# Optimization experiments

Measured on AMD Instinct MI355X. Metric: run time of the kernel, lower is better.

The kernel has to match this reference:

```python
import jax, jax.numpy as jnp
import numpy as np
from math import log

MODEL_DIM = 512
NUM_HEADS = 8
DIM_HEAD = 64
INNER = NUM_HEADS * DIM_HEAD
B, L = 8, 1024
EPS = 1e-5


def setup_inputs() -> dict:
    key = jax.random.key(0)
    ks = jax.random.split(key, 9)
    x = jax.random.normal(ks[0], (B, L, MODEL_DIM), dtype=jnp.float32)
    gamma = jnp.ones((MODEL_DIM,), jnp.float32)
    beta = jnp.zeros((MODEL_DIM,), jnp.float32)
    w_qkv = jax.random.normal(ks[1], (3 * INNER, MODEL_DIM), jnp.float32) * (MODEL_DIM ** -0.5)
    b_qkv = jnp.zeros((3 * INNER,), jnp.float32)
    w_pos = jax.random.normal(ks[2], (INNER, MODEL_DIM), jnp.float32) * (MODEL_DIM ** -0.5)
    w_out = jax.random.normal(ks[3], (MODEL_DIM, INNER), jnp.float32) * (INNER ** -0.5)
    b_out = jnp.zeros((MODEL_DIM,), jnp.float32)
    # xavier_uniform for (num_heads, dim_head)
    bound = (6.0 / (NUM_HEADS + DIM_HEAD)) ** 0.5
    u_bias = jax.random.uniform(ks[4], (NUM_HEADS, DIM_HEAD), jnp.float32, -bound, bound)
    v_bias = jax.random.uniform(ks[5], (NUM_HEADS, DIM_HEAD), jnp.float32, -bound, bound)
    return {"x": x, "gamma": gamma, "beta": beta, "w_qkv": w_qkv, "b_qkv": b_qkv,
            "w_pos": w_pos, "w_out": w_out, "b_out": b_out, "u_bias": u_bias, "v_bias": v_bias}


def _rel_pos_emb(seq_len, d):
    # (L, D): (i - j) scaled by sinusoid frequencies, then cos on even cols, sin on odd cols
    rel = (jnp.arange(seq_len, dtype=jnp.float32)[:, None]
           - jnp.arange(d, dtype=jnp.float32)[None, :])
    freqs = jnp.exp(-jnp.arange(0, 2 * d, 2, dtype=jnp.float32) * (log(10000.0) / MODEL_DIM))
    angle = rel * freqs[None, :]
    even = (jnp.arange(d) % 2) == 0
    return jnp.where(even[None, :], jnp.cos(angle), jnp.sin(angle))  # (L, D)


def reference(x, gamma, beta, w_qkv, b_qkv, w_pos, w_out, b_out, u_bias, v_bias):
    b, l, d = x.shape
    h, dh = NUM_HEADS, DIM_HEAD
    # LayerNorm
    mu = jnp.mean(x, axis=-1, keepdims=True)
    var = jnp.mean(jnp.square(x - mu), axis=-1, keepdims=True)
    xn = (x - mu) * jax.lax.rsqrt(var + EPS) * gamma + beta
    # relative position embedding, identical per batch element
    pe = _rel_pos_emb(l, d)                      # (L, D)
    pos = (pe @ w_pos.T).reshape(l, h, dh)       # (L, H, Dh)
    pos = jnp.transpose(pos, (1, 0, 2))          # (H, L, Dh)
    # qkv
    qkv = xn @ w_qkv.T + b_qkv                   # (B, L, 3*inner)
    q, k, v = jnp.split(qkv, 3, axis=-1)
    def to_heads(t):
        return jnp.transpose(t.reshape(b, l, h, dh), (0, 2, 1, 3))  # (B,H,L,Dh)
    q, k, v = to_heads(q), to_heads(k), to_heads(v)
    scale = dh ** -0.5
    content = jnp.einsum('bhld,bhmd->bhlm', q + u_bias[None, :, None, :], k)
    pos_score = jnp.einsum('bhld,hmd->bhlm', q + v_bias[None, :, None, :], pos)
    attn = jax.nn.softmax((content + pos_score) * scale, axis=-1)
    out = jnp.einsum('bhlm,bhmd->bhld', attn, v)
    out = jnp.transpose(out, (0, 2, 1, 3)).reshape(b, l, h * dh)
    return out @ w_out.T + b_out  # dropout p=0.0 -> identity
```

## Files before the change

### kernel.cpp

```cpp
#include <hip/hip_runtime.h>
#include <math.h>

static constexpr int Bn = 8, Ln = 1024, Dm = 512, Hn = 8, DhN = 64;

typedef short bf16x8 __attribute__((ext_vector_type(8)));
typedef float f32x4 __attribute__((ext_vector_type(4)));
typedef _Float16 f16x4 __attribute__((ext_vector_type(4)));
typedef _Float16 f16x8 __attribute__((ext_vector_type(8)));
typedef unsigned int u32x4 __attribute__((ext_vector_type(4)));

#define QSCALE 0.1803368801111137f

static __device__ __forceinline__ unsigned short f2b(float f) {
  union { float f; unsigned int u; } x;
  x.f = f;
  unsigned int u = x.u;
  unsigned int r = (u + 0x7FFFu + ((u >> 16) & 1u)) >> 16;
  return (unsigned short)r;
}
static __device__ __forceinline__ float b2f(unsigned short u) {
  union { unsigned int u; float f; } x;
  x.u = ((unsigned int)u) << 16;
  return x.f;
}

#define GLDS16(g, l)                                                        \
  __builtin_amdgcn_global_load_lds((const __attribute__((address_space(1))) void*)(g), \
                                   (__attribute__((address_space(3))) void*)(l), 16, 0, 0)

__global__ __launch_bounds__(256) void prep1(const float* __restrict__ x,
                                             const float* __restrict__ gamma,
                                             const float* __restrict__ beta,
                                             unsigned short* __restrict__ xn,
                                             unsigned short* __restrict__ pe,
                                             const float* __restrict__ wq, unsigned short* __restrict__ wqb,
                                             const float* __restrict__ wp, unsigned short* __restrict__ wpb,
                                             const float* __restrict__ wo, unsigned short* __restrict__ wob) {
  int b = blockIdx.x;
  int t = threadIdx.x;
  if (b < 8192) {
    const float2 v = *(const float2*)(x + (size_t)b * Dm + t * 2);
    float s = v.x + v.y;
    float sq = v.x * v.x + v.y * v.y;
#pragma unroll
    for (int off = 32; off > 0; off >>= 1) {
      s += __shfl_down(s, off);
      sq += __shfl_down(sq, off);
    }
    __shared__ float red[8];
    int wave = t >> 6, lane = t & 63;
    if (lane == 0) { red[wave * 2] = s; red[wave * 2 + 1] = sq; }
    __syncthreads();
    float S = red[0] + red[2] + red[4] + red[6];
    float SQ = red[1] + red[3] + red[5] + red[7];
    float mu = S * (1.0f / Dm);
    float var = SQ * (1.0f / Dm) - mu * mu;
    float rstd = rsqrtf(var + 1e-5f);
    int c = t * 2;
    ushort2 o;
    o.x = f2b((v.x - mu) * rstd * gamma[c] + beta[c]);
    o.y = f2b((v.y - mu) * rstd * gamma[c + 1] + beta[c + 1]);
    *(ushort2*)(xn + (size_t)b * Dm + c) = o;
  } else if (b < 10240) {
    int idx = (b - 8192) * 256 + t;
    int l = idx >> 9, k = idx & 511;
    float freq = expf(-0.0359778921f * (float)k);
    float angle = (float)(l - k) * freq;
    pe[idx] = f2b((k & 1) ? sinf(angle) : cosf(angle));
  } else {
    int cb = b - 10240;
    const float* src;
    unsigned short* dst;
    int off;
    if (cb < 768) { src = wq; dst = wqb; off = cb; }
    else if (cb < 1024) { src = wp; dst = wpb; off = cb - 768; }
    else { src = wo; dst = wob; off = cb - 1024; }
    int i = off * 256 + t;
    float4 v = *(const float4*)(src + (size_t)i * 4);
    ushort4 o;
    o.x = f2b(v.x); o.y = f2b(v.y); o.z = f2b(v.z); o.w = f2b(v.w);
    *(ushort4*)(dst + (size_t)i * 4) = o;
  }
}

__global__ __launch_bounds__(256, 8) void gemm_mfma(const unsigned short* __restrict__ Ain,
                                                    const unsigned short* __restrict__ Bwin,
                                                    const float* __restrict__ biasin,
                                                    float* __restrict__ outfin,
                                                    unsigned short* __restrict__ oq,
                                                    unsigned short* __restrict__ ok,
                                                    unsigned short* __restrict__ ov,
                                                    const unsigned short* __restrict__ A2,
                                                    const unsigned short* __restrict__ B2,
                                                    float* __restrict__ outf2,
                                                    int K, int mode) {
  int by = blockIdx.y, bx = blockIdx.x;
  if (by < 128) {
    int NBX = gridDim.x;
    int lid = by * NBX + bx;
    int i = lid >> 3;
    by = (lid & 7) * 16 + i / NBX;
    bx = i % NBX;
  }
  const unsigned short* A = Ain;
  const unsigned short* Bw = Bwin;
  const float* bias = biasin;
  float* outf = outfin;
  if (by >= 128) {
    if (bx >= 8) return;
    A = A2; Bw = B2; bias = nullptr; outf = outf2; mode = 1; by -= 128;
  }
  __shared__ alignas(16) unsigned short As[64 * 64];
  __shared__ alignas(16) unsigned short Bs[64 * 64];
  const int t = threadIdx.x;
  const int lane = t & 63, w = t >> 6;
  const int c = lane & 15, q8 = lane >> 4;
  const int wm = (w & 1) * 32, wn = (w >> 1) * 32;
  const int m0 = by * 64, n0 = bx * 64;

  f32x4 acc[2][2];
#pragma unroll
  for (int i = 0; i < 2; ++i)
#pragma unroll
    for (int j = 0; j < 2; ++j) acc[i][j] = (f32x4){0.f, 0.f, 0.f, 0.f};

  const int srow = lane >> 3;
  const int sgr = (lane & 7) ^ srow;

  for (int k0 = 0; k0 < K; k0 += 64) {
    __syncthreads();
#pragma unroll
    for (int j = 0; j < 2; ++j) {
      int r = j * 32 + w * 8 + srow;
      GLDS16(A + (size_t)(m0 + r) * K + k0 + sgr * 8, As + (j * 256 + w * 64 + lane) * 8);
      GLDS16(Bw + (size_t)(n0 + r) * K + k0 + sgr * 8, Bs + (j * 256 + w * 64 + lane) * 8);
    }
    __syncthreads();
#pragma unroll
    for (int kk = 0; kk < 2; ++kk) {
      bf16x8 a[2], b[2];
      const int q = kk * 4 + q8;
#pragma unroll
      for (int i = 0; i < 2; ++i) {
        int r = wm + i * 16 + c;
        a[i] = *(const bf16x8*)&As[(r * 8 + (q ^ (r & 7))) * 8];
      }
#pragma unroll
      for (int j = 0; j < 2; ++j) {
        int r = wn + j * 16 + c;
        b[j] = *(const bf16x8*)&Bs[(r * 8 + (q ^ (r & 7))) * 8];
      }
#pragma unroll
      for (int i = 0; i < 2; ++i)
#pragma unroll
        for (int j = 0; j < 2; ++j)
          acc[i][j] = __builtin_amdgcn_mfma_f32_16x16x32_bf16(a[i], b[j], acc[i][j], 0, 0, 0);
    }
  }
#pragma unroll
  for (int i = 0; i < 2; ++i) {
#pragma unroll
    for (int r = 0; r < 4; ++r) {
      int m = m0 + wm + i * 16 + q8 * 4 + r;
#pragma unroll
      for (int j = 0; j < 2; ++j) {
        int n = n0 + wn + j * 16 + c;
        float val = acc[i][j][r] + (bias ? bias[n] : 0.0f);
        if (mode == 0) {
          int part = n >> 9, h = (n >> 6) & 7, dh = n & 63;
          int bb = m >> 10, l = m & 1023;
          size_t idx = (size_t)((bb * 8 + h) * 1024 + l) * 64 + dh;
          if (part == 0) {
            oq[idx] = f2b(val * QSCALE);
          } else if (part == 1) {
            ok[idx] = f2b(val);
          } else {
            union { _Float16 h; unsigned short u; } cv;
            cv.h = (_Float16)val;
            ov[idx] = cv.u;
          }
        } else if (mode == 1) {
          int h = n >> 6, dh = n & 63;
          outf[(size_t)(h * 1024 + m) * 64 + dh] = val;
        } else {
          outf[(size_t)m * 512 + n] = val;
        }
      }
    }
  }
}

__global__ __launch_bounds__(256) void prep2(unsigned short* __restrict__ kbuf,
                                             const float* __restrict__ pos,
                                             const float* __restrict__ ub,
                                             const float* __restrict__ vbb,
                                             float* __restrict__ biasout,
                                             const unsigned short* __restrict__ v,
                                             unsigned short* __restrict__ vt) {
  int b = blockIdx.x;
  int t = threadIdx.x;
  if (b < 16384) {
    int wave = t >> 6, lane = t & 63;
    int g = b * 4 + wave;
    int h = (g >> 10) & 7;
    int m = g & 1023;
    float kv = b2f(kbuf[(size_t)g * 64 + lane]);
    float pv = pos[(size_t)(h * 1024 + m) * 64 + lane];
    float val = ub[h * 64 + lane] * kv + vbb[h * 64 + lane] * pv;
#pragma unroll
    for (int off = 32; off > 0; off >>= 1) val += __shfl_down(val, off);
    if (lane == 0) biasout[g] = val * QSCALE;
    kbuf[(size_t)g * 64 + lane] = f2b(kv + pv);
  } else {
    __shared__ unsigned short Ts[64 * 68];
    int bb = b - 16384;
    int bh = bb >> 4, lt = bb & 15;
    const unsigned short* vg = v + (size_t)bh * 65536 + lt * 4096;
#pragma unroll
    for (int s = 0; s < 4; ++s) {
      int idx = t + s * 256;
      int r = idx >> 4, c4 = (idx & 15) << 2;
      *(ushort4*)&Ts[r * 68 + c4] = *(const ushort4*)(vg + r * 64 + c4);
    }
    __syncthreads();
#pragma unroll
    for (int s = 0; s < 4; ++s) {
      int idx = t + s * 256;
      int d = idx >> 4, l4 = (idx & 15) << 2;
      ushort4 o;
      o.x = Ts[(l4 + 0) * 68 + d];
      o.y = Ts[(l4 + 1) * 68 + d];
      o.z = Ts[(l4 + 2) * 68 + d];
      o.w = Ts[(l4 + 3) * 68 + d];
      int pb = ((l4 >> 5) & 1) * 32 + ((l4 >> 2) & 3) * 8 + ((l4 >> 4) & 1) * 4;
      *(ushort4*)(vt + (size_t)bh * 65536 + d * 1024 + lt * 64 + pb) = o;
    }
  }
}

__global__ __launch_bounds__(256, 2) void flash_mfma(const unsigned short* __restrict__ qbf,
                                                     const unsigned short* __restrict__ kbf,
                                                     const unsigned short* __restrict__ vt,
                                                     const float* __restrict__ bias,
                                                     unsigned short* __restrict__ attn_out) {
  __shared__ alignas(16) unsigned short Ks[2][64 * 64];
  __shared__ alignas(16) unsigned short Vs[2][64 * 64];
  __shared__ alignas(16) float Bls[1024];
  const int t = threadIdx.x;
  const int lane = t & 63, w = t >> 6;
  const int c = lane & 15, q8 = lane >> 4;
  const int cc7 = c & 7;
  const int lid = blockIdx.x + (blockIdx.y << 3);
  const int bh = ((lid & 7) << 3) + ((lid >> 3) & 7);
  const int qt = lid >> 6;
  const unsigned short* qg = qbf + (size_t)bh * 65536;
  const unsigned short* kg = kbf + (size_t)bh * 65536;
  const unsigned short* vg = vt + (size_t)bh * 65536;
  const float* bg = bias + (size_t)bh * 1024;

  GLDS16(bg + t * 4, Bls + t * 4);

  bf16x8 bq[2][2];
#pragma unroll
  for (int g = 0; g < 2; ++g) {
    int qlg = qt * 128 + g * 64 + w * 16 + c;
    bq[g][0] = *(const bf16x8*)(qg + (size_t)qlg * 64 + q8 * 8);
    bq[g][1] = *(const bf16x8*)(qg + (size_t)qlg * 64 + 32 + q8 * 8);
  }

  float m_st[2] = {-INFINITY, -INFINITY};
  float l_st[2] = {0.0f, 0.0f};
  f32x4 o[2][4];
#pragma unroll
  for (int g = 0; g < 2; ++g)
#pragma unroll
    for (int i = 0; i < 4; ++i) o[g][i] = (f32x4){0.f, 0.f, 0.f, 0.f};

  const int srow = lane >> 3;
  const int sgr = (lane & 7) ^ srow;
  const int r0 = w * 16 + srow;

  u32x4 pk[2][2], pv[2][2];
#pragma unroll
  for (int h = 0; h < 2; ++h)
#pragma unroll
    for (int j = 0; j < 2; ++j) {
      int r = r0 + j * 8;
      pk[h][j] = *(const u32x4*)(kg + (size_t)(h * 64 + r) * 64 + sgr * 8);
      pv[h][j] = *(const u32x4*)(vg + (size_t)r * 1024 + h * 64 + sgr * 8);
    }

  for (int it = 0; it < 8; ++it) {
    __syncthreads();
#pragma unroll
    for (int h = 0; h < 2; ++h)
#pragma unroll
      for (int j = 0; j < 2; ++j) {
        int r = r0 + j * 8;
        *(u32x4*)&Ks[h][(r * 8 + (lane & 7)) * 8] = pk[h][j];
        *(u32x4*)&Vs[h][(r * 8 + (lane & 7)) * 8] = pv[h][j];
      }
    __syncthreads();
    if (it < 7) {
#pragma unroll
      for (int h = 0; h < 2; ++h)
#pragma unroll
        for (int j = 0; j < 2; ++j) {
          int r = r0 + j * 8;
          pk[h][j] = *(const u32x4*)(kg + (size_t)((it + 1) * 128 + h * 64 + r) * 64 + sgr * 8);
          pv[h][j] = *(const u32x4*)(vg + (size_t)r * 1024 + (it + 1) * 128 + h * 64 + sgr * 8);
        }
    }

    f32x4 sc[2][2][4];
#pragma unroll
    for (int h = 0; h < 2; ++h) {
#pragma unroll
      for (int nt = 0; nt < 4; ++nt) {
        f32x4 ci = *(const f32x4*)&Bls[it * 128 + h * 64 + nt * 16 + q8 * 4];
        const int row = nt * 16 + c;
        bf16x8 ak0 = *(const bf16x8*)&Ks[h][(row * 8 + (q8 ^ cc7)) * 8];
        bf16x8 ak1 = *(const bf16x8*)&Ks[h][(row * 8 + ((q8 + 4) ^ cc7)) * 8];
#pragma unroll
        for (int g = 0; g < 2; ++g) {
          f32x4 z = __builtin_amdgcn_mfma_f32_16x16x32_bf16(ak0, bq[g][0], ci, 0, 0, 0);
          sc[g][h][nt] = __builtin_amdgcn_mfma_f32_16x16x32_bf16(ak1, bq[g][1], z, 0, 0, 0);
        }
      }
    }
    float mx[2];
#pragma unroll
    for (int g = 0; g < 2; ++g) {
      float m = sc[g][0][0][0];
#pragma unroll
      for (int h = 0; h < 2; ++h)
#pragma unroll
        for (int nt = 0; nt < 4; ++nt)
#pragma unroll
          for (int r = 0; r < 4; ++r) m = fmaxf(m, sc[g][h][nt][r]);
      mx[g] = m;
    }
    {
      float s0 = __shfl_xor(mx[0], 16);
      float s1 = __shfl_xor(mx[1], 16);
      mx[0] = fmaxf(mx[0], s0);
      mx[1] = fmaxf(mx[1], s1);
      s0 = __shfl_xor(mx[0], 32);
      s1 = __shfl_xor(mx[1], 32);
      mx[0] = fmaxf(mx[0], s0);
      mx[1] = fmaxf(mx[1], s1);
    }
    f16x8 pf8[2][2][2];
#pragma unroll
    for (int g = 0; g < 2; ++g) {
      float mn = fmaxf(m_st[g], mx[g]);
      float al = __builtin_amdgcn_exp2f(m_st[g] - mn);
      float su = 0.0f;
#pragma unroll
      for (int h = 0; h < 2; ++h)
#pragma unroll
        for (int nt = 0; nt < 4; ++nt)
#pragma unroll
          for (int r = 0; r < 4; ++r) {
            float p = __builtin_amdgcn_exp2f(sc[g][h][nt][r] - mn);
            su += p;
            pf8[g][h][nt >> 1][((nt & 1) << 2) | r] = (_Float16)p;
          }
      l_st[g] = l_st[g] * al + su;
      m_st[g] = mn;
#pragma unroll
      for (int i = 0; i < 4; ++i) o[g][i] *= al;
    }
#pragma unroll
    for (int i = 0; i < 4; ++i) {
      const int row = i * 16 + c;
#pragma unroll
      for (int h = 0; h < 2; ++h) {
        f16x8 va = *(const f16x8*)&Vs[h][(row * 8 + (q8 ^ cc7)) * 8];
        f16x8 vb = *(const f16x8*)&Vs[h][(row * 8 + ((4 + q8) ^ cc7)) * 8];
#pragma unroll
        for (int g = 0; g < 2; ++g) {
          o[g][i] = __builtin_amdgcn_mfma_f32_16x16x32_f16(va, pf8[g][h][0], o[g][i], 0, 0, 0);
          o[g][i] = __builtin_amdgcn_mfma_f32_16x16x32_f16(vb, pf8[g][h][1], o[g][i], 0, 0, 0);
        }
      }
    }
  }
  float lt0 = l_st[0], lt1 = l_st[1];
  {
    float s0 = __shfl_xor(lt0, 16);
    float s1 = __shfl_xor(lt1, 16);
    lt0 += s0; lt1 += s1;
    s0 = __shfl_xor(lt0, 32);
    s1 = __shfl_xor(lt1, 32);
    lt0 += s0; lt1 += s1;
  }
  const int bidx = bh >> 3, h = bh & 7;
#pragma unroll
  for (int g = 0; g < 2; ++g) {
    int qlg = qt * 128 + g * 64 + w * 16 + c;
    float inv = 1.0f / (g == 0 ? lt0 : lt1);
    size_t base = (size_t)(bidx * 1024 + qlg) * 512 + h * 64;
#pragma unroll
    for (int i = 0; i < 4; ++i) {
      ushort4 ov4;
      ov4.x = f2b(o[g][i][0] * inv);
      ov4.y = f2b(o[g][i][1] * inv);
      ov4.z = f2b(o[g][i][2] * inv);
      ov4.w = f2b(o[g][i][3] * inv);
      *(ushort4*)(attn_out + base + i * 16 + q8 * 4) = ov4;
    }
  }
}

extern "C" void kernel_launch(void* const* d_in, const int* in_sizes, int n_in,
                              void* d_out, int out_size, void* d_ws, size_t ws_size,
                              hipStream_t stream) {
  const float* x      = (const float*)d_in[0];
  const float* gamma  = (const float*)d_in[1];
  const float* beta   = (const float*)d_in[2];
  const float* w_qkv  = (const float*)d_in[3];
  const float* b_qkv  = (const float*)d_in[4];
  const float* w_pos  = (const float*)d_in[5];
  const float* w_out  = (const float*)d_in[6];
  const float* b_out  = (const float*)d_in[7];
  const float* u_bias = (const float*)d_in[8];
  const float* v_bias = (const float*)d_in[9];
  float* out = (float*)d_out;

  unsigned short* wsu = (unsigned short*)d_ws;
  unsigned short* xnb   = wsu;
  unsigned short* peb   = wsu + 4194304;
  unsigned short* wqkvb = wsu + 4718592;
  unsigned short* wposb = wsu + 5505024;
  unsigned short* woutb = wsu + 5767168;
  unsigned short* qbf   = wsu + 6291456;
  unsigned short* kbf   = wsu + 10485760;
  unsigned short* vbf   = wsu + 14680064;
  unsigned short* vtb   = wsu + 18874368;
  unsigned short* attnb = wsu + 23068672;
  float* posb  = (float*)(wsu + 27262976);
  float* biasb = (float*)(wsu + 28311552);

  prep1<<<11520, 256, 0, stream>>>(x, gamma, beta, xnb, peb,
                                   w_qkv, wqkvb, w_pos, wposb, w_out, woutb);
  gemm_mfma<<<dim3(24, 144), 256, 0, stream>>>(xnb, wqkvb, b_qkv, nullptr, qbf, kbf, vbf,
                                               peb, wposb, posb, 512, 0);
  prep2<<<17408, 256, 0, stream>>>(kbf, posb, u_bias, v_bias, biasb, vbf, vtb);
  flash_mfma<<<dim3(8, 64), 256, 0, stream>>>(qbf, kbf, vtb, biasb, attnb);
  gemm_mfma<<<dim3(8, 128), 256, 0, stream>>>(attnb, woutb, b_out, out, nullptr, nullptr, nullptr,
                                              nullptr, nullptr, nullptr, 512, 2);
}
```

Baseline: 171.5 us.

## Halve flash attention query tile per block to raise occupancy and add setprio

Each flash attention block now processes 64 query rows instead of 128, doubling the grid and raising launch bounds to allow four blocks per CU. Per-thread state (two query groups) collapses to one, reducing register pressure. MFMA sections are wrapped with s_setprio to favour matrix issue across waves. This trades doubled K/V and bias loads per query row for more resident waves and better latency hiding.

```diff
diff --git a/kernel.cpp b/kernel.cpp
--- a/kernel.cpp
+++ b/kernel.cpp
@@ -238,7 +238,7 @@
   }
 }
 
-__global__ __launch_bounds__(256, 2) void flash_mfma(const unsigned short* __restrict__ qbf,
+__global__ __launch_bounds__(256, 4) void flash_mfma(const unsigned short* __restrict__ qbf,
                                                      const unsigned short* __restrict__ kbf,
                                                      const unsigned short* __restrict__ vt,
                                                      const float* __restrict__ bias,
@@ -250,7 +250,7 @@
   const int lane = t & 63, w = t >> 6;
   const int c = lane & 15, q8 = lane >> 4;
   const int cc7 = c & 7;
-  const int lid = blockIdx.x + (blockIdx.y << 3);
+  const int lid = blockIdx.x + (blockIdx.y << 4);
   const int bh = ((lid & 7) << 3) + ((lid >> 3) & 7);
   const int qt = lid >> 6;
   const unsigned short* qg = qbf + (size_t)bh * 65536;
@@ -260,21 +260,15 @@
 
   GLDS16(bg + t * 4, Bls + t * 4);
 
-  bf16x8 bq[2][2];
-#pragma unroll
-  for (int g = 0; g < 2; ++g) {
-    int qlg = qt * 128 + g * 64 + w * 16 + c;
-    bq[g][0] = *(const bf16x8*)(qg + (size_t)qlg * 64 + q8 * 8);
-    bq[g][1] = *(const bf16x8*)(qg + (size_t)qlg * 64 + 32 + q8 * 8);
-  }
-
-  float m_st[2] = {-INFINITY, -INFINITY};
-  float l_st[2] = {0.0f, 0.0f};
-  f32x4 o[2][4];
-#pragma unroll
-  for (int g = 0; g < 2; ++g)
-#pragma unroll
-    for (int i = 0; i < 4; ++i) o[g][i] = (f32x4){0.f, 0.f, 0.f, 0.f};
+  const int qlg = qt * 64 + w * 16 + c;
+  bf16x8 bq0 = *(const bf16x8*)(qg + (size_t)qlg * 64 + q8 * 8);
+  bf16x8 bq1 = *(const bf16x8*)(qg + (size_t)qlg * 64 + 32 + q8 * 8);
+
+  float m_st = -INFINITY;
+  float l_st = 0.0f;
+  f32x4 o[4];
+#pragma unroll
+  for (int i = 0; i < 4; ++i) o[i] = (f32x4){0.f, 0.f, 0.f, 0.f};
 
   const int srow = lane >> 3;
   const int sgr = (lane & 7) ^ srow;
@@ -312,7 +306,8 @@
         }
     }
 
-    f32x4 sc[2][2][4];
+    f32x4 sc[2][4];
+    __builtin_amdgcn_s_setprio(1);
 #pragma unroll
     for (int h = 0; h < 2; ++h) {
 #pragma unroll
@@ -321,56 +316,41 @@
         const int row = nt * 16 + c;
         bf16x8 ak0 = *(const bf16x8*)&Ks[h][(row * 8 + (q8 ^ cc7)) * 8];
         bf16x8 ak1 = *(const bf16x8*)&Ks[h][(row * 8 + ((q8 + 4) ^ cc7)) * 8];
-#pragma unroll
-        for (int g = 0; g < 2; ++g) {
-          f32x4 z = __builtin_amdgcn_mfma_f32_16x16x32_bf16(ak0, bq[g][0], ci, 0, 0, 0);
-          sc[g][h][nt] = __builtin_amdgcn_mfma_f32_16x16x32_bf16(ak1, bq[g][1], z, 0, 0, 0);
-        }
-      }
-    }
-    float mx[2];
-#pragma unroll
-    for (int g = 0; g < 2; ++g) {
-      float m = sc[g][0][0][0];
+        f32x4 z = __builtin_amdgcn_mfma_f32_16x16x32_bf16(ak0, bq0, ci, 0, 0, 0);
+        sc[h][nt] = __builtin_amdgcn_mfma_f32_16x16x32_bf16(ak1, bq1, z, 0, 0, 0);
+      }
+    }
+    __builtin_amdgcn_s_setprio(0);
+    float mx = sc[0][0][0];
+#pragma unroll
+    for (int h = 0; h < 2; ++h)
+#pragma unroll
+      for (int nt = 0; nt < 4; ++nt)
+#pragma unroll
+        for (int r = 0; r < 4; ++r) mx = fmaxf(mx, sc[h][nt][r]);
+    mx = fmaxf(mx, __shfl_xor(mx, 16));
+    mx = fmaxf(mx, __shfl_xor(mx, 32));
+    f16x8 pf8[2][2];
+    {
+      float mn = fmaxf(m_st, mx);
+      float al = __builtin_amdgcn_exp2f(m_st - mn);
+      float su = 0.0f;
 #pragma unroll
       for (int h = 0; h < 2; ++h)
 #pragma unroll
         for (int nt = 0; nt < 4; ++nt)
 #pragma unroll
-          for (int r = 0; r < 4; ++r) m = fmaxf(m, sc[g][h][nt][r]);
-      mx[g] = m;
-    }
-    {
-      float s0 = __shfl_xor(mx[0], 16);
-      float s1 = __shfl_xor(mx[1], 16);
-      mx[0] = fmaxf(mx[0], s0);
-      mx[1] = fmaxf(mx[1], s1);
-      s0 = __shfl_xor(mx[0], 32);
-      s1 = __shfl_xor(mx[1], 32);
-      mx[0] = fmaxf(mx[0], s0);
-      mx[1] = fmaxf(mx[1], s1);
-    }
-    f16x8 pf8[2][2][2];
-#pragma unroll
-    for (int g = 0; g < 2; ++g) {
-      float mn = fmaxf(m_st[g], mx[g]);
-      float al = __builtin_amdgcn_exp2f(m_st[g] - mn);
-      float su = 0.0f;
-#pragma unroll
-      for (int h = 0; h < 2; ++h)
-#pragma unroll
-        for (int nt = 0; nt < 4; ++nt)
-#pragma unroll
           for (int r = 0; r < 4; ++r) {
-            float p = __builtin_amdgcn_exp2f(sc[g][h][nt][r] - mn);
+            float p = __builtin_amdgcn_exp2f(sc[h][nt][r] - mn);
             su += p;
-            pf8[g][h][nt >> 1][((nt & 1) << 2) | r] = (_Float16)p;
+            pf8[h][nt >> 1][((nt & 1) << 2) | r] = (_Float16)p;
           }
-      l_st[g] = l_st[g] * al + su;
-      m_st[g] = mn;
-#pragma unroll
-      for (int i = 0; i < 4; ++i) o[g][i] *= al;
-    }
+      l_st = l_st * al + su;
+      m_st = mn;
+#pragma unroll
+      for (int i = 0; i < 4; ++i) o[i] *= al;
+    }
+    __builtin_amdgcn_s_setprio(1);
 #pragma unroll
     for (int i = 0; i < 4; ++i) {
       const int row = i * 16 + c;
@@ -378,38 +358,26 @@
       for (int h = 0; h < 2; ++h) {
         f16x8 va = *(const f16x8*)&Vs[h][(row * 8 + (q8 ^ cc7)) * 8];
         f16x8 vb = *(const f16x8*)&Vs[h][(row * 8 + ((4 + q8) ^ cc7)) * 8];
-#pragma unroll
-        for (int g = 0; g < 2; ++g) {
-          o[g][i] = __builtin_amdgcn_mfma_f32_16x16x32_f16(va, pf8[g][h][0], o[g][i], 0, 0, 0);
-          o[g][i] = __builtin_amdgcn_mfma_f32_16x16x32_f16(vb, pf8[g][h][1], o[g][i], 0, 0, 0);
-        }
-      }
-    }
-  }
-  float lt0 = l_st[0], lt1 = l_st[1];
-  {
-    float s0 = __shfl_xor(lt0, 16);
-    float s1 = __shfl_xor(lt1, 16);
-    lt0 += s0; lt1 += s1;
-    s0 = __shfl_xor(lt0, 32);
-    s1 = __shfl_xor(lt1, 32);
-    lt0 += s0; lt1 += s1;
-  }
+        o[i] = __builtin_amdgcn_mfma_f32_16x16x32_f16(va, pf8[h][0], o[i], 0, 0, 0);
+        o[i] = __builtin_amdgcn_mfma_f32_16x16x32_f16(vb, pf8[h][1], o[i], 0, 0, 0);
+      }
+    }
+    __builtin_amdgcn_s_setprio(0);
+  }
+  float lt = l_st;
+  lt += __shfl_xor(lt, 16);
+  lt += __shfl_xor(lt, 32);
   const int bidx = bh >> 3, h = bh & 7;
-#pragma unroll
-  for (int g = 0; g < 2; ++g) {
-    int qlg = qt * 128 + g * 64 + w * 16 + c;
-    float inv = 1.0f / (g == 0 ? lt0 : lt1);
-    size_t base = (size_t)(bidx * 1024 + qlg) * 512 + h * 64;
-#pragma unroll
-    for (int i = 0; i < 4; ++i) {
-      ushort4 ov4;
-      ov4.x = f2b(o[g][i][0] * inv);
-      ov4.y = f2b(o[g][i][1] * inv);
-      ov4.z = f2b(o[g][i][2] * inv);
-      ov4.w = f2b(o[g][i][3] * inv);
-      *(ushort4*)(attn_out + base + i * 16 + q8 * 4) = ov4;
-    }
+  float inv = 1.0f / lt;
+  size_t base = (size_t)(bidx * 1024 + qlg) * 512 + h * 64;
+#pragma unroll
+  for (int i = 0; i < 4; ++i) {
+    ushort4 ov4;
+    ov4.x = f2b(o[i][0] * inv);
+    ov4.y = f2b(o[i][1] * inv);
+    ov4.z = f2b(o[i][2] * inv);
+    ov4.w = f2b(o[i][3] * inv);
+    *(ushort4*)(attn_out + base + i * 16 + q8 * 4) = ov4;
   }
 }
 
@@ -447,7 +415,7 @@
   gemm_mfma<<<dim3(24, 144), 256, 0, stream>>>(xnb, wqkvb, b_qkv, nullptr, qbf, kbf, vbf,
                                                peb, wposb, posb, 512, 0);
   prep2<<<17408, 256, 0, stream>>>(kbf, posb, u_bias, v_bias, biasb, vbf, vtb);
-  flash_mfma<<<dim3(8, 64), 256, 0, stream>>>(qbf, kbf, vtb, biasb, attnb);
+  flash_mfma<<<dim3(16, 64), 256, 0, stream>>>(qbf, kbf, vtb, biasb, attnb);
   gemm_mfma<<<dim3(8, 128), 256, 0, stream>>>(attnb, woutb, b_out, out, nullptr, nullptr, nullptr,
                                               nullptr, nullptr, nullptr, 512, 2);
 }
```

After: 173.6 us. No clear change (+1.2%).

## Double-buffer GEMM LDS tiles to overlap global loads with MFMA

Applied to the files above, without the earlier changes.

Converts the projection GEMM's single LDS tile into a ping-pong pair, issuing the direct-to-LDS loads for the next K tile before computing on the current one, with explicit vmcnt waits and barriers. The goal is to hide global-memory latency behind MFMA work instead of stalling on it every iteration. This doubles LDS use per block to 32KB and lowers the launch-bounds occupancy hint from 8 to 5, so fewer blocks fit per CU. It also relies on hand-placed vmcnt counts being correct.

```diff
diff --git a/kernel.cpp b/kernel.cpp
--- a/kernel.cpp
+++ b/kernel.cpp
@@ -83,7 +83,7 @@
   }
 }
 
-__global__ __launch_bounds__(256, 8) void gemm_mfma(const unsigned short* __restrict__ Ain,
+__global__ __launch_bounds__(256, 5) void gemm_mfma(const unsigned short* __restrict__ Ain,
                                                     const unsigned short* __restrict__ Bwin,
                                                     const float* __restrict__ biasin,
                                                     float* __restrict__ outfin,
@@ -110,8 +110,8 @@
     if (bx >= 8) return;
     A = A2; Bw = B2; bias = nullptr; outf = outf2; mode = 1; by -= 128;
   }
-  __shared__ alignas(16) unsigned short As[64 * 64];
-  __shared__ alignas(16) unsigned short Bs[64 * 64];
+  __shared__ alignas(16) unsigned short As[2][64 * 64];
+  __shared__ alignas(16) unsigned short Bs[2][64 * 64];
   const int t = threadIdx.x;
   const int lane = t & 63, w = t >> 6;
   const int c = lane & 15, q8 = lane >> 4;
@@ -127,15 +127,33 @@
   const int srow = lane >> 3;
   const int sgr = (lane & 7) ^ srow;
 
-  for (int k0 = 0; k0 < K; k0 += 64) {
-    __syncthreads();
-#pragma unroll
-    for (int j = 0; j < 2; ++j) {
-      int r = j * 32 + w * 8 + srow;
-      GLDS16(A + (size_t)(m0 + r) * K + k0 + sgr * 8, As + (j * 256 + w * 64 + lane) * 8);
-      GLDS16(Bw + (size_t)(n0 + r) * K + k0 + sgr * 8, Bs + (j * 256 + w * 64 + lane) * 8);
-    }
-    __syncthreads();
+#define STAGE_GEMM(buf, k0s)                                                              \
+  do {                                                                                    \
+    _Pragma("unroll")                                                                     \
+    for (int j = 0; j < 2; ++j) {                                                         \
+      int r = j * 32 + w * 8 + srow;                                                      \
+      GLDS16(A + (size_t)(m0 + r) * K + (k0s) + sgr * 8,                                  \
+             &As[buf][(j * 256 + w * 64 + lane) * 8]);                                    \
+      GLDS16(Bw + (size_t)(n0 + r) * K + (k0s) + sgr * 8,                                 \
+             &Bs[buf][(j * 256 + w * 64 + lane) * 8]);                                    \
+    }                                                                                     \
+  } while (0)
+
+  const int NT = K >> 6;
+  STAGE_GEMM(0, 0);
+  for (int it = 0; it < NT; ++it) {
+    const int cur = it & 1;
+    __builtin_amdgcn_s_barrier();
+    __builtin_amdgcn_sched_barrier(0);
+    if (it + 1 < NT) {
+      STAGE_GEMM(cur ^ 1, (it + 1) << 6);
+      asm volatile("s_waitcnt vmcnt(4)" ::: "memory");
+    } else {
+      asm volatile("s_waitcnt vmcnt(0)" ::: "memory");
+    }
+    __builtin_amdgcn_sched_barrier(0);
+    __builtin_amdgcn_s_barrier();
+    __builtin_amdgcn_sched_barrier(0);
 #pragma unroll
     for (int kk = 0; kk < 2; ++kk) {
       bf16x8 a[2], b[2];
@@ -143,12 +161,12 @@
 #pragma unroll
       for (int i = 0; i < 2; ++i) {
         int r = wm + i * 16 + c;
-        a[i] = *(const bf16x8*)&As[(r * 8 + (q ^ (r & 7))) * 8];
+        a[i] = *(const bf16x8*)&As[cur][(r * 8 + (q ^ (r & 7))) * 8];
       }
 #pragma unroll
       for (int j = 0; j < 2; ++j) {
         int r = wn + j * 16 + c;
-        b[j] = *(const bf16x8*)&Bs[(r * 8 + (q ^ (r & 7))) * 8];
+        b[j] = *(const bf16x8*)&Bs[cur][(r * 8 + (q ^ (r & 7))) * 8];
       }
 #pragma unroll
       for (int i = 0; i < 2; ++i)
@@ -157,6 +175,7 @@
           acc[i][j] = __builtin_amdgcn_mfma_f32_16x16x32_bf16(a[i], b[j], acc[i][j], 0, 0, 0);
     }
   }
+#undef STAGE_GEMM
 #pragma unroll
   for (int i = 0; i < 2; ++i) {
 #pragma unroll
```

Measured after the change: 182.2 us. +6.3%, slower.

## Load K/V tiles directly from global memory into MFMA operands, dropping LDS staging

Applied to the files above, without the earlier changes.

The flash attention kernel no longer stages K, V and the bias row through shared memory with a register prefetch and two barriers per iteration. Each wave now reads its MFMA operands straight from global memory, relying on L1/L2 caching. Launch bounds rise to 3 blocks per CU to use the freed LDS and registers. The cost is four waves redundantly fetching the same K/V data through the cache hierarchy, and global-load latency that is no longer hidden by the explicit prefetch.

```diff
diff --git a/kernel.cpp b/kernel.cpp
--- a/kernel.cpp
+++ b/kernel.cpp
@@ -238,18 +238,14 @@
   }
 }
 
-__global__ __launch_bounds__(256, 2) void flash_mfma(const unsigned short* __restrict__ qbf,
+__global__ __launch_bounds__(256, 3) void flash_mfma(const unsigned short* __restrict__ qbf,
                                                      const unsigned short* __restrict__ kbf,
                                                      const unsigned short* __restrict__ vt,
                                                      const float* __restrict__ bias,
                                                      unsigned short* __restrict__ attn_out) {
-  __shared__ alignas(16) unsigned short Ks[2][64 * 64];
-  __shared__ alignas(16) unsigned short Vs[2][64 * 64];
-  __shared__ alignas(16) float Bls[1024];
   const int t = threadIdx.x;
   const int lane = t & 63, w = t >> 6;
   const int c = lane & 15, q8 = lane >> 4;
-  const int cc7 = c & 7;
   const int lid = blockIdx.x + (blockIdx.y << 3);
   const int bh = ((lid & 7) << 3) + ((lid >> 3) & 7);
   const int qt = lid >> 6;
@@ -258,8 +254,6 @@
   const unsigned short* vg = vt + (size_t)bh * 65536;
   const float* bg = bias + (size_t)bh * 1024;
 
-  GLDS16(bg + t * 4, Bls + t * 4);
-
   bf16x8 bq[2][2];
 #pragma unroll
   for (int g = 0; g < 2; ++g) {
@@ -276,51 +270,16 @@
 #pragma unroll
     for (int i = 0; i < 4; ++i) o[g][i] = (f32x4){0.f, 0.f, 0.f, 0.f};
 
-  const int srow = lane >> 3;
-  const int sgr = (lane & 7) ^ srow;
-  const int r0 = w * 16 + srow;
-
-  u32x4 pk[2][2], pv[2][2];
-#pragma unroll
-  for (int h = 0; h < 2; ++h)
-#pragma unroll
-    for (int j = 0; j < 2; ++j) {
-      int r = r0 + j * 8;
-      pk[h][j] = *(const u32x4*)(kg + (size_t)(h * 64 + r) * 64 + sgr * 8);
-      pv[h][j] = *(const u32x4*)(vg + (size_t)r * 1024 + h * 64 + sgr * 8);
-    }
-
   for (int it = 0; it < 8; ++it) {
-    __syncthreads();
-#pragma unroll
-    for (int h = 0; h < 2; ++h)
-#pragma unroll
-      for (int j = 0; j < 2; ++j) {
-        int r = r0 + j * 8;
-        *(u32x4*)&Ks[h][(r * 8 + (lane & 7)) * 8] = pk[h][j];
-        *(u32x4*)&Vs[h][(r * 8 + (lane & 7)) * 8] = pv[h][j];
-      }
-    __syncthreads();
-    if (it < 7) {
-#pragma unroll
-      for (int h = 0; h < 2; ++h)
-#pragma unroll
-        for (int j = 0; j < 2; ++j) {
-          int r = r0 + j * 8;
-          pk[h][j] = *(const u32x4*)(kg + (size_t)((it + 1) * 128 + h * 64 + r) * 64 + sgr * 8);
-          pv[h][j] = *(const u32x4*)(vg + (size_t)r * 1024 + (it + 1) * 128 + h * 64 + sgr * 8);
-        }
-    }
-
     f32x4 sc[2][2][4];
 #pragma unroll
     for (int h = 0; h < 2; ++h) {
 #pragma unroll
       for (int nt = 0; nt < 4; ++nt) {
-        f32x4 ci = *(const f32x4*)&Bls[it * 128 + h * 64 + nt * 16 + q8 * 4];
-        const int row = nt * 16 + c;
-        bf16x8 ak0 = *(const bf16x8*)&Ks[h][(row * 8 + (q8 ^ cc7)) * 8];
-        bf16x8 ak1 = *(const bf16x8*)&Ks[h][(row * 8 + ((q8 + 4) ^ cc7)) * 8];
+        const int krow = it * 128 + h * 64 + nt * 16 + c;
+        f32x4 ci = *(const f32x4*)(bg + it * 128 + h * 64 + nt * 16 + q8 * 4);
+        bf16x8 ak0 = *(const bf16x8*)(kg + (size_t)krow * 64 + q8 * 8);
+        bf16x8 ak1 = *(const bf16x8*)(kg + (size_t)krow * 64 + 32 + q8 * 8);
 #pragma unroll
         for (int g = 0; g < 2; ++g) {
           f32x4 z = __builtin_amdgcn_mfma_f32_16x16x32_bf16(ak0, bq[g][0], ci, 0, 0, 0);
@@ -373,11 +332,11 @@
     }
 #pragma unroll
     for (int i = 0; i < 4; ++i) {
-      const int row = i * 16 + c;
+      const int vrow = i * 16 + c;
 #pragma unroll
       for (int h = 0; h < 2; ++h) {
-        f16x8 va = *(const f16x8*)&Vs[h][(row * 8 + (q8 ^ cc7)) * 8];
-        f16x8 vb = *(const f16x8*)&Vs[h][(row * 8 + ((4 + q8) ^ cc7)) * 8];
+        f16x8 va = *(const f16x8*)(vg + (size_t)vrow * 1024 + it * 128 + h * 64 + q8 * 8);
+        f16x8 vb = *(const f16x8*)(vg + (size_t)vrow * 1024 + it * 128 + h * 64 + 32 + q8 * 8);
 #pragma unroll
         for (int g = 0; g < 2; ++g) {
           o[g][i] = __builtin_amdgcn_mfma_f32_16x16x32_f16(va, pf8[g][h][0], o[g][i], 0, 0, 0);
```

New measurement: 205.5 us. +19.9%, slower.
